# Optimization experiments

Hardware: AMD Instinct MI355X
Metric: run time of the kernel (lower is better)

The kernel has to match this reference:

```python
import jax, jax.numpy as jnp
import numpy as np

B, W, IN, H, Z, D, OUT, K = 256, 128, 128, 1024, 128, 1024, 128, 3


def _gru_cell(h, x, Wih, Whh, bih, bhh):
    # torch nn.GRU single-layer cell, gate order (r, z, n)
    gi = x @ Wih.T + bih
    gh = h @ Whh.T + bhh
    ir, iz, inn = jnp.split(gi, 3, axis=-1)
    hr, hz, hn = jnp.split(gh, 3, axis=-1)
    r = jax.nn.sigmoid(ir + hr)
    u = jax.nn.sigmoid(iz + hz)
    n = jnp.tanh(inn + r * hn)
    return (1.0 - u) * n + u * h


def setup_inputs():
    key = jax.random.key(0)
    ks = iter(jax.random.split(key, 40))

    def w(shape, fanin):
        return jax.random.normal(next(ks), shape, jnp.float32) / np.float32(np.sqrt(fanin))

    return dict(
        x=jax.random.normal(next(ks), (B, W, IN), jnp.float32),
        eps_q=jax.random.uniform(next(ks), (B, W, Z), jnp.float32),
        eps_p=jax.random.uniform(next(ks), (B, W, OUT), jnp.float32),
        Wih_q=w((3 * H, IN), IN), Whh_q=w((3 * H, H), H),
        bih_q=jnp.zeros(3 * H, jnp.float32), bhh_q=jnp.zeros(3 * H, jnp.float32),
        Wd_q=w((D, Z + H), Z + H), bd_q=jnp.zeros(D, jnp.float32),
        Wmu_q=w((Z, D), D), bmu_q=jnp.zeros(Z, jnp.float32),
        Wsig_q=w((Z, D), D), bsig_q=jnp.zeros(Z, jnp.float32),
        Wp=w((K, Z, Z), Z), bp=jnp.zeros((K, Z), jnp.float32),
        up=0.1 * jax.random.normal(next(ks), (K,), jnp.float32),
        Wlg=w((Z, Z), Z), blg=jnp.zeros(Z, jnp.float32),
        Wih_p=w((3 * H, Z), Z), Whh_p=w((3 * H, H), H),
        bih_p=jnp.zeros(3 * H, jnp.float32), bhh_p=jnp.zeros(3 * H, jnp.float32),
        Wd_p=w((D, H), H), bd_p=jnp.zeros(D, jnp.float32),
        Wmu_p=w((OUT, D), D), bmu_p=jnp.zeros(OUT, jnp.float32),
        Wsig_p=w((OUT, D), D), bsig_p=jnp.zeros(OUT, jnp.float32),
    )


def _forward(x, eps_q, eps_p, Wih_q, Whh_q, bih_q, bhh_q, Wd_q, bd_q, Wmu_q, bmu_q,
             Wsig_q, bsig_q, Wp, bp, up, Wlg, blg, Wih_p, Whh_p, bih_p, bhh_p,
             Wd_p, bd_p, Wmu_p, bmu_p, Wsig_p, bsig_p):
    Bsz = x.shape[0]

    # ---- Qnet: sequential encoder with planar flows ----
    def q_step(carry, inp):
        e, z_prev = carry
        x_t, eps_t = inp  # [B,IN], [B,Z]
        e = _gru_cell(e, x_t, Wih_q, Whh_q, bih_q, bhh_q)
        d = jnp.concatenate([z_prev, e], axis=-1) @ Wd_q.T + bd_q
        mu = d @ Wmu_q.T + bmu_q
        logvar = jax.nn.softplus(d @ Wsig_q.T + bsig_q)
        z = mu + jnp.exp(0.5 * logvar) * eps_t
        for k in range(K):  # planar normalizing flows: z + u * tanh(Wz + b)
            z = z + up[k] * jnp.tanh(z @ Wp[k].T + bp[k])
        return (e, z), (z, mu, logvar)

    e0 = jnp.zeros((Bsz, H), x.dtype)
    z0 = jnp.zeros((Bsz, Z), x.dtype)
    _, (z_seq, mu_seq, lv_seq) = jax.lax.scan(
        q_step, (e0, z0), (jnp.swapaxes(x, 0, 1), jnp.swapaxes(eps_q, 0, 1)))

    # ---- Pnet: sequential decoder ----
    def p_step(d_t, inp):
        z_t, eps_t = inp
        zt = z_t @ Wlg.T + blg  # LGSSM linear
        d_t = _gru_cell(d_t, zt, Wih_p, Whh_p, bih_p, bhh_p)
        dd = d_t @ Wd_p.T + bd_p
        mu = dd @ Wmu_p.T + bmu_p
        sigma = jax.nn.softplus(dd @ Wsig_p.T + bsig_p)
        return d_t, mu + sigma * eps_t

    d0 = jnp.zeros((Bsz, H), x.dtype)
    _, out_seq = jax.lax.scan(p_step, d0, (z_seq, jnp.swapaxes(eps_p, 0, 1)))

    return (jnp.swapaxes(out_seq, 0, 1),
            jnp.swapaxes(mu_seq, 0, 1),
            jnp.swapaxes(lv_seq, 0, 1))


def reference(x, eps_q, eps_p, Wih_q, Whh_q, bih_q, bhh_q, Wd_q, bd_q, Wmu_q, bmu_q,
              Wsig_q, bsig_q, Wp, bp, up, Wlg, blg, Wih_p, Whh_p, bih_p, bhh_p,
              Wd_p, bd_p, Wmu_p, bmu_p, Wsig_p, bsig_p):
    return _forward(x, eps_q, eps_p, Wih_q, Whh_q, bih_q, bhh_q, Wd_q, bd_q, Wmu_q,
                    bmu_q, Wsig_q, bsig_q, Wp, bp, up, Wlg, blg, Wih_p, Whh_p,
                    bih_p, bhh_p, Wd_p, bd_p, Wmu_p, bmu_p, Wsig_p, bsig_p)
```

## Files before the change

### kernel.cpp

```cpp
#include <hip/hip_runtime.h>


typedef __bf16 bf16;
typedef __bf16 bf16x4 __attribute__((ext_vector_type(4)));
typedef __bf16 bf16x8 __attribute__((ext_vector_type(8)));
typedef float  f32x4  __attribute__((ext_vector_type(4)));
typedef unsigned long long u64;
typedef unsigned u32;

static constexpr int CB   = 256;
static constexpr int CW   = 128;
static constexpr int CIN  = 128;
static constexpr int CH   = 1024;
static constexpr int CZ   = 128;
static constexpr int CD   = 1024;
static constexpr int COUT = 128;

static constexpr int APITCH     = 1160;
static constexpr int ABUF_BYTES = 16 * APITCH * 2;
static constexpr int REDN       = 8 * 16 * 17;
static constexpr int RED2_BYTES = 2 * REDN * 4;
static constexpr int FLOW_BYTES = (2 * CZ + 2 * 2 * CZ) * 4;
static constexpr int SMEM_BYTES = ABUF_BYTES + RED2_BYTES + FLOW_BYTES;

#define DEV static __device__ __forceinline__

DEV float sigmoidf_(float x) { return 1.0f / (1.0f + expf(-x)); }
DEV float softplusf_(float x) { return x > 20.0f ? x : log1pf(expf(x)); }
DEV bf16x8 ldfrag(const bf16* p) { return *reinterpret_cast<const bf16x8*>(p); }

#define MFMA(a, b, c) __builtin_amdgcn_mfma_f32_16x16x32_bf16((a), (b), (c), 0, 0, 0)

DEV u64 lda8(const void* p) {
    return __hip_atomic_load((const u64*)p, __ATOMIC_RELAXED, __HIP_MEMORY_SCOPE_AGENT);
}
DEV u32 lda4(const void* p) {
    return __hip_atomic_load((const u32*)p, __ATOMIC_RELAXED, __HIP_MEMORY_SCOPE_AGENT);
}
DEV void sta4(void* p, u32 v) {
    __hip_atomic_store((u32*)p, v, __ATOMIC_RELAXED, __HIP_MEMORY_SCOPE_AGENT);
}
DEV bf16x8 ld_act16(const bf16* p) {
    union { u64 u[2]; bf16x8 v; } r;
    r.u[0] = lda8(p);
    r.u[1] = lda8((const char*)p + 8);
    return r.v;
}
DEV u32 pk2(float a, float b) {
    union { bf16 h[2]; u32 u; } r;
    r.h[0] = (bf16)a; r.h[1] = (bf16)b;
    return r.u;
}

struct Prm {
    const float *eps_q, *eps_p;
    const float *bih_q, *bhh_q, *bd_q, *bmu_q, *bsig_q;
    const float *Wp, *bp, *up, *Wlg, *blg;
    const float *bih_p, *bhh_p, *bd_p, *bmu_p, *bsig_p;
    const bf16 *x_b, *Wih_qb, *Whh_qb, *Wd_qb, *Wmu_qb, *Wsg_qb;
    const bf16 *Wih_pb, *Whh_pb, *Wd_pb, *Wmu_pb, *Wsg_pb;
    float *e_f0, *e_f1; bf16 *e_b0, *e_b1;
    float *d_f0, *d_f1; bf16 *d_b0, *d_b1;
    float *ztmp_f;
    bf16 *dvec_b, *ddvec_b;
    bf16 *zflow;
    bf16 *ztlg;
    u32 *barQ, *barP, *zbar;
    float *out_o, *out_mu, *out_lv;
};

DEV void gbar_h(u32* bar, int wgl, u32 k)
{
    asm volatile("s_waitcnt vmcnt(0)" ::: "memory");
    __syncthreads();
    if (threadIdx.x == 0)
        __hip_atomic_store(&bar[wgl], k, __ATOMIC_RELAXED, __HIP_MEMORY_SCOPE_AGENT);
    if (threadIdx.x < 128) {
        while (__hip_atomic_load(&bar[threadIdx.x], __ATOMIC_RELAXED,
                                 __HIP_MEMORY_SCOPE_AGENT) < k)
            __builtin_amdgcn_s_sleep(1);
    }
    __syncthreads();
}

__global__ void k_cvt(const float* __restrict__ src, bf16* __restrict__ dst, int n)
{
    int i = (blockIdx.x * blockDim.x + threadIdx.x) * 4;
    if (i < n) {
        float4 v = *reinterpret_cast<const float4*>(src + i);
        bf16x4 o;
        o[0] = (bf16)v.x; o[1] = (bf16)v.y; o[2] = (bf16)v.z; o[3] = (bf16)v.w;
        *reinterpret_cast<bf16x4*>(dst + i) = o;
    }
}

DEV void stage_act(bf16* abuf, int tid, int r0,
                   const bf16* __restrict__ head, long hs, int K1, int hagent,
                   const bf16* __restrict__ body, long bs)
{
    const int CHN = (K1 + CH) >> 3;
    const int TOT = 16 * CHN;
    for (int idx = tid; idx < TOT; idx += 512) {
        const int row = idx / CHN;
        const int k = (idx - row * CHN) * 8;
        bf16x8 v;
        if (k < K1) {
            const bf16* s = head + (long)(r0 + row) * hs + k;
            v = hagent ? ld_act16(s) : ldfrag(s);
        } else {
            v = ld_act16(body + (long)(r0 + row) * bs + (k - K1));
        }
        *reinterpret_cast<bf16x8*>(abuf + (long)row * APITCH + k) = v;
    }
    __syncthreads();
}

DEV void gru_compute(const Prm& p, const bf16* abuf, int r0, int n0,
                     int lane, int wave,
                     const bf16* __restrict__ Wih, const bf16* __restrict__ Whh,
                     const float* __restrict__ bih, const float* __restrict__ bhh,
                     const float* __restrict__ Efin,
                     float* __restrict__ Efo, bf16* __restrict__ Ebo)
{
    const int lr = lane & 15, lkE = (lane >> 4) * 8;
    const int c = n0 + wave * 16 + lr;
    const bf16* arow = abuf + (long)lr * APITCH;

    f32x4 acc[4] = {};
#pragma unroll 4
    for (int k = 0; k < CIN; k += 32) {
        bf16x8 a = *reinterpret_cast<const bf16x8*>(arow + k + lkE);
#pragma unroll
        for (int g = 0; g < 3; ++g) {
            bf16x8 b = ldfrag(Wih + ((long)g * CH + c) * CIN + k + lkE);
            const int grp = (g == 2) ? 2 : g;
            acc[grp] = MFMA(a, b, acc[grp]);
        }
    }
#pragma unroll 4
    for (int k = 0; k < CH; k += 32) {
        bf16x8 a = *reinterpret_cast<const bf16x8*>(arow + CIN + k + lkE);
#pragma unroll
        for (int g = 0; g < 3; ++g) {
            bf16x8 b = ldfrag(Whh + ((long)g * CH + c) * CH + k + lkE);
            const int grp = (g == 2) ? 3 : g;
            acc[grp] = MFMA(a, b, acc[grp]);
        }
    }

    const float b0r = bih[c] + bhh[c];
    const float b0z = bih[CH + c] + bhh[CH + c];
    const float bin = bih[2 * CH + c];
    const float bhn = bhh[2 * CH + c];
    const int rbase = r0 + (lane >> 4) * 4;
#pragma unroll
    for (int i = 0; i < 4; ++i) {
        const int row = rbase + i;
        float gr = acc[0][i] + b0r;
        float gz = acc[1][i] + b0z;
        float gi = acc[2][i] + bin;
        float gh = acc[3][i] + bhn;
        float r = sigmoidf_(gr);
        float u = sigmoidf_(gz);
        float n = tanhf(gi + r * gh);
        float en = (1.0f - u) * n + u * Efin[(long)row * CH + c];
        Efo[(long)row * CH + c] = en;
        float vB = __shfl_xor(en, 1);
        if (!(lane & 1))
            sta4(Ebo + (long)row * CH + c, pk2(en, vB));
    }
}

DEV void lin_compute(const bf16* abuf, int r0, int n0, int lane, int wave, int Ktot,
                     const bf16* __restrict__ W,
                     const float* __restrict__ bias, bf16* __restrict__ Out)
{
    const int lr = lane & 15, lkE = (lane >> 4) * 8;
    const int c = n0 + wave * 16 + lr;
    const bf16* arow = abuf + (long)lr * APITCH;
    const bf16* wrow = W + (long)c * Ktot;

    f32x4 acc = {};
#pragma unroll 4
    for (int k = 0; k < CH; k += 32) {
        bf16x8 a = *reinterpret_cast<const bf16x8*>(arow + (Ktot - CH) + k + lkE);
        bf16x8 b = ldfrag(wrow + (Ktot - CH) + k + lkE);
        acc = MFMA(a, b, acc);
    }
    if (Ktot > CH) {
#pragma unroll 4
        for (int k = 0; k < CZ; k += 32) {
            bf16x8 a = *reinterpret_cast<const bf16x8*>(arow + k + lkE);
            bf16x8 b = ldfrag(wrow + k + lkE);
            acc = MFMA(a, b, acc);
        }
    }

    const float bb = bias[c];
    const int rbase = r0 + (lane >> 4) * 4;
#pragma unroll
    for (int i = 0; i < 4; ++i) {
        float v = acc[i] + bb;
        float vB = __shfl_xor(v, 1);
        if (!(lane & 1))
            sta4(Out + (long)(rbase + i) * CD + c, pk2(v, vB));
    }
}

template <int MODE>
DEV void phase_tail2(const Prm& p, int t, int wgl, int tid, int lane, int wave,
                     float* Ra, float* Rs, const bf16* __restrict__ A,
                     const bf16* __restrict__ Wa, const bf16* __restrict__ Wb,
                     const float* __restrict__ ba, const float* __restrict__ bb)
{
    const int lr = lane & 15, lkE = (lane >> 4) * 8;
    const int mb = (wgl >> 3) << 4;
    const int nb = (wgl & 7) << 4;
    f32x4 am = {}, as = {};
    const int k0 = wave * 128;
#pragma unroll
    for (int kk = 0; kk < 128; kk += 32) {
        const int k = k0 + kk;
        bf16x8 a  = ld_act16(A + (long)(mb + lr) * CD + k + lkE);
        bf16x8 bm = ldfrag(Wa + (long)(nb + lr) * CD + k + lkE);
        bf16x8 bs = ldfrag(Wb + (long)(nb + lr) * CD + k + lkE);
        am = MFMA(a, bm, am);
        as = MFMA(a, bs, as);
    }
    __syncthreads();
#pragma unroll
    for (int i = 0; i < 4; ++i) {
        Ra[(wave * 16 + (lane >> 4) * 4 + i) * 17 + lr] = am[i];
        Rs[(wave * 16 + (lane >> 4) * 4 + i) * 17 + lr] = as[i];
    }
    __syncthreads();
    if (tid < 256) {
        const int trow = tid >> 4, tcol = tid & 15;
        float vm = 0.f, vs = 0.f;
#pragma unroll
        for (int w = 0; w < 8; ++w) {
            vm += Ra[(w * 16 + trow) * 17 + tcol];
            vs += Rs[(w * 16 + trow) * 17 + tcol];
        }
        const int row = mb + trow, col = nb + tcol;
        if constexpr (MODE == 0) {
            float mu = vm + ba[col];
            float lv = softplusf_(vs + bb[col]);
            float e  = p.eps_q[(long)row * CW * CZ + (long)t * CZ + col];
            float z  = mu + expf(0.5f * lv) * e;
            p.out_mu[(long)row * CW * CZ + (long)t * CZ + col] = mu;
            p.out_lv[(long)row * CW * CZ + (long)t * CZ + col] = lv;
            sta4(p.ztmp_f + (long)row * CZ + col, __float_as_uint(z));
        } else {
            float m  = vm + ba[col];
            float sg = softplusf_(vs + bb[col]);
            float e  = p.eps_p[(long)row * CW * COUT + (long)t * COUT + col];
            p.out_o[(long)row * CW * COUT + (long)t * COUT + col] = m + sg * e;
        }
    }
}

DEV void phase_flows2(const Prm& p, int wgl, int tid, int t, float* zl, float* ps)
{
    const int rg = tid >> 8;
    const int sub = tid & 255;
    const int c = sub & 127, half = sub >> 7;
    const int row = wgl * 2 + rg;
    float* zrow = zl + rg * CZ;
    float* pall = ps + rg * 2 * CZ;

    if (half == 0)
        zrow[c] = __uint_as_float(lda4(p.ztmp_f + (long)row * CZ + c));
    __syncthreads();

#pragma unroll 1
    for (int kf = 0; kf < 3; ++kf) {
        const float* wr = p.Wp + ((long)kf * CZ + c) * CZ + half * 64;
        const float* zh = zrow + half * 64;
        float s = 0.f;
#pragma unroll
        for (int j = 0; j < 64; j += 4) {
            float4 w = *reinterpret_cast<const float4*>(wr + j);
            s += zh[j] * w.x + zh[j + 1] * w.y + zh[j + 2] * w.z + zh[j + 3] * w.w;
        }
        pall[half * CZ + c] = s;
        __syncthreads();
        if (half == 0) {
            float sf = pall[c] + pall[CZ + c] + p.bp[kf * CZ + c];
            zrow[c] += p.up[kf] * tanhf(sf);
        }
        __syncthreads();
    }
    {
        const float* wr = p.Wlg + (long)c * CZ + half * 64;
        const float* zh = zrow + half * 64;
        float s = 0.f;
#pragma unroll
        for (int j = 0; j < 64; j += 4) {
            float4 w = *reinterpret_cast<const float4*>(wr + j);
            s += zh[j] * w.x + zh[j + 1] * w.y + zh[j + 2] * w.z + zh[j + 3] * w.w;
        }
        pall[half * CZ + c] = s;
        __syncthreads();
        if (half == 0) {
            float zt = pall[c] + pall[CZ + c] + p.blg[c];
            float ztB = __shfl_xor(zt, 1);
            if (!(c & 1)) {
                sta4(p.ztlg  + ((size_t)t * CB + row) * CZ + c, pk2(zt, ztB));
                sta4(p.zflow + ((size_t)(t + 1) * CB + row) * CZ + c,
                     pk2(zrow[c], zrow[c + 1]));
            }
        }
    }
}

__launch_bounds__(512)
__global__ void mega(Prm p)
{
    extern __shared__ char smem[];
    bf16*  abuf = (bf16*)smem;
    float* Ra   = (float*)(smem + ABUF_BYTES);
    float* Rs   = Ra + REDN;
    float* ZLp  = (float*)(smem + ABUF_BYTES + RED2_BYTES);
    float* PSp  = ZLp + 2 * CZ;

    const int wg = blockIdx.x, tid = threadIdx.x;
    const int lane = tid & 63, wave = tid >> 6;
    const bool isQ = wg < 128;
    const int wgl = isQ ? wg : wg - 128;
    const int r0 = (wgl >> 3) * 16;
    const int n0 = (wgl & 7) * 128;

    if (isQ) {
        u32 bk = 0;
#pragma unroll 1
        for (int t = 0; t < CW; ++t) {
            const int bi = t & 1;
            const bf16*  eb_i = bi ? p.e_b1 : p.e_b0;
            const float* ef_i = bi ? p.e_f1 : p.e_f0;
            bf16*  eb_o = bi ? p.e_b0 : p.e_b1;
            float* ef_o = bi ? p.e_f0 : p.e_f1;

            stage_act(abuf, tid, r0, p.x_b + (long)t * CIN, (long)CW * CIN, CIN, 0,
                      eb_i, CH);
            gru_compute(p, abuf, r0, n0, lane, wave, p.Wih_qb, p.Whh_qb,
                        p.bih_q, p.bhh_q, ef_i, ef_o, eb_o);
            gbar_h(p.barQ, wgl, ++bk);
            stage_act(abuf, tid, r0, p.zflow + (size_t)t * CB * CZ, CZ, CZ, 1,
                      eb_o, CH);
            lin_compute(abuf, r0, n0, lane, wave, CZ + CH, p.Wd_qb, p.bd_q, p.dvec_b);
            gbar_h(p.barQ, wgl, ++bk);
            phase_tail2<0>(p, t, wgl, tid, lane, wave, Ra, Rs,
                           p.dvec_b, p.Wmu_qb, p.Wsg_qb, p.bmu_q, p.bsig_q);
            gbar_h(p.barQ, wgl, ++bk);
            phase_flows2(p, wgl, tid, t, ZLp, PSp);
            asm volatile("s_waitcnt vmcnt(0)" ::: "memory");
            __syncthreads();
            if (tid == 0)
                __hip_atomic_store(&p.zbar[wgl], (u32)(t + 1),
                                   __ATOMIC_RELAXED, __HIP_MEMORY_SCOPE_AGENT);
            __syncthreads();
        }
    } else {
        u32 bk = 0;
#pragma unroll 1
        for (int t = 0; t < CW; ++t) {
            if (tid < 128) {
                while (__hip_atomic_load(&p.zbar[tid], __ATOMIC_RELAXED,
                                         __HIP_MEMORY_SCOPE_AGENT) < (u32)(t + 1))
                    __builtin_amdgcn_s_sleep(2);
            }
            __syncthreads();

            const int bi = t & 1;
            const bf16*  db_i = bi ? p.d_b1 : p.d_b0;
            const float* df_i = bi ? p.d_f1 : p.d_f0;
            bf16*  db_o = bi ? p.d_b0 : p.d_b1;
            float* df_o = bi ? p.d_f0 : p.d_f1;

            stage_act(abuf, tid, r0, p.ztlg + (size_t)t * CB * CZ, CZ, CZ, 1,
                      db_i, CH);
            gru_compute(p, abuf, r0, n0, lane, wave, p.Wih_pb, p.Whh_pb,
                        p.bih_p, p.bhh_p, df_i, df_o, db_o);
            gbar_h(p.barP, wgl, ++bk);
            stage_act(abuf, tid, r0, nullptr, 0, 0, 0, db_o, CH);
            lin_compute(abuf, r0, n0, lane, wave, CH, p.Wd_pb, p.bd_p, p.ddvec_b);
            gbar_h(p.barP, wgl, ++bk);
            phase_tail2<1>(p, t, wgl, tid, lane, wave, Ra, Rs,
                           p.ddvec_b, p.Wmu_pb, p.Wsg_pb, p.bmu_p, p.bsig_p);
        }
    }
}

extern "C" void kernel_launch(void* const* d_in, const int* in_sizes, int n_in,
                              void* d_out, int out_size, void* d_ws, size_t ws_size,
                              hipStream_t stream)
{
    Prm p;
    const float* x      = (const float*)d_in[0];
    p.eps_q  = (const float*)d_in[1];
    p.eps_p  = (const float*)d_in[2];
    const float* Wih_q  = (const float*)d_in[3];
    const float* Whh_q  = (const float*)d_in[4];
    p.bih_q  = (const float*)d_in[5];
    p.bhh_q  = (const float*)d_in[6];
    const float* Wd_q   = (const float*)d_in[7];
    p.bd_q   = (const float*)d_in[8];
    const float* Wmu_q  = (const float*)d_in[9];
    p.bmu_q  = (const float*)d_in[10];
    const float* Wsig_q = (const float*)d_in[11];
    p.bsig_q = (const float*)d_in[12];
    p.Wp     = (const float*)d_in[13];
    p.bp     = (const float*)d_in[14];
    p.up     = (const float*)d_in[15];
    p.Wlg    = (const float*)d_in[16];
    p.blg    = (const float*)d_in[17];
    const float* Wih_p  = (const float*)d_in[18];
    const float* Whh_p  = (const float*)d_in[19];
    p.bih_p  = (const float*)d_in[20];
    p.bhh_p  = (const float*)d_in[21];
    const float* Wd_p   = (const float*)d_in[22];
    p.bd_p   = (const float*)d_in[23];
    const float* Wmu_p  = (const float*)d_in[24];
    p.bmu_p  = (const float*)d_in[25];
    const float* Wsig_p = (const float*)d_in[26];
    p.bsig_p = (const float*)d_in[27];

    p.out_o  = (float*)d_out;
    p.out_mu = p.out_o + (size_t)CB * CW * COUT;
    p.out_lv = p.out_mu + (size_t)CB * CW * CZ;

    char* wp_ = (char*)d_ws;
    auto carve = [&](size_t bytes) -> void* {
        void* q = (void*)wp_;
        wp_ += (bytes + 255) & ~(size_t)255;
        return q;
    };
    p.e_f0 = (float*)carve((size_t)CB * CH * 4);
    p.e_f1 = (float*)carve((size_t)CB * CH * 4);
    p.e_b0 = (bf16*)carve((size_t)CB * CH * 2);
    p.e_b1 = (bf16*)carve((size_t)CB * CH * 2);
    p.d_f0 = (float*)carve((size_t)CB * CH * 4);
    p.d_f1 = (float*)carve((size_t)CB * CH * 4);
    p.d_b0 = (bf16*)carve((size_t)CB * CH * 2);
    p.d_b1 = (bf16*)carve((size_t)CB * CH * 2);
    p.ztmp_f  = (float*)carve((size_t)CB * CZ * 4);
    p.dvec_b  = (bf16*)carve((size_t)CB * CD * 2);
    p.ddvec_b = (bf16*)carve((size_t)CB * CD * 2);
    p.zflow   = (bf16*)carve((size_t)(CW + 1) * CB * CZ * 2);
    p.ztlg    = (bf16*)carve((size_t)CW * CB * CZ * 2);
    p.barQ    = (u32*)carve(512);
    p.barP    = (u32*)carve(512);
    p.zbar    = (u32*)carve(512);
    bf16* x_b    = (bf16*)carve((size_t)CB * CW * CIN * 2);
    bf16* Wih_qb = (bf16*)carve((size_t)3 * CH * CIN * 2);
    bf16* Whh_qb = (bf16*)carve((size_t)3 * CH * CH * 2);
    bf16* Wd_qb  = (bf16*)carve((size_t)CD * (CZ + CH) * 2);
    bf16* Wmu_qb = (bf16*)carve((size_t)CZ * CD * 2);
    bf16* Wsg_qb = (bf16*)carve((size_t)CZ * CD * 2);
    bf16* Wih_pb = (bf16*)carve((size_t)3 * CH * CZ * 2);
    bf16* Whh_pb = (bf16*)carve((size_t)3 * CH * CH * 2);
    bf16* Wd_pb  = (bf16*)carve((size_t)CD * CH * 2);
    bf16* Wmu_pb = (bf16*)carve((size_t)COUT * CD * 2);
    bf16* Wsg_pb = (bf16*)carve((size_t)COUT * CD * 2);
    p.x_b = x_b;       p.Wih_qb = Wih_qb; p.Whh_qb = Whh_qb;
    p.Wd_qb = Wd_qb;   p.Wmu_qb = Wmu_qb; p.Wsg_qb = Wsg_qb;
    p.Wih_pb = Wih_pb; p.Whh_pb = Whh_pb; p.Wd_pb = Wd_pb;
    p.Wmu_pb = Wmu_pb; p.Wsg_pb = Wsg_pb;

    hipMemsetAsync(p.e_f0, 0, (size_t)CB * CH * 4, stream);
    hipMemsetAsync(p.e_b0, 0, (size_t)CB * CH * 2, stream);
    hipMemsetAsync(p.d_f0, 0, (size_t)CB * CH * 4, stream);
    hipMemsetAsync(p.d_b0, 0, (size_t)CB * CH * 2, stream);
    hipMemsetAsync(p.zflow, 0, (size_t)CB * CZ * 2, stream);
    hipMemsetAsync(p.barQ, 0, 512, stream);
    hipMemsetAsync(p.barP, 0, 512, stream);
    hipMemsetAsync(p.zbar, 0, 512, stream);

    auto cvt = [&](const float* s, bf16* d, size_t n) {
        k_cvt<<<dim3((unsigned)((n / 4 + 255) / 256)), dim3(256), 0, stream>>>(s, d, (int)n);
    };
    cvt(x,      x_b,    (size_t)CB * CW * CIN);
    cvt(Wih_q,  Wih_qb, (size_t)3 * CH * CIN);
    cvt(Whh_q,  Whh_qb, (size_t)3 * CH * CH);
    cvt(Wd_q,   Wd_qb,  (size_t)CD * (CZ + CH));
    cvt(Wmu_q,  Wmu_qb, (size_t)CZ * CD);
    cvt(Wsig_q, Wsg_qb, (size_t)CZ * CD);
    cvt(Wih_p,  Wih_pb, (size_t)3 * CH * CZ);
    cvt(Whh_p,  Whh_pb, (size_t)3 * CH * CH);
    cvt(Wd_p,   Wd_pb,  (size_t)CD * CH);
    cvt(Wmu_p,  Wmu_pb, (size_t)COUT * CD);
    cvt(Wsig_p, Wsg_pb, (size_t)COUT * CD);

    mega<<<dim3(256), dim3(512), SMEM_BYTES, stream>>>(p);
}
```

Before: 9.720 ms.

## Use per-timestep write-once activation buffers so reads can use cached loads

When the workspace is large enough, hidden states, intermediate vectors, z samples and LGSSM outputs are kept in per-timestep slices rather than ping-pong buffers. Each slice is then written only once, so consumers can use ordinary cached fragment loads instead of coherent agent-scope loads. This is meant to cut the latency of cross-workgroup activation reads inside the persistent recurrent kernel. In exchange it uses much more workspace memory, falls back to the old path when the workspace is small, and relies on the cached reads never seeing stale lines. The convert kernel also switches to packed stores.

Result: slower. 10.68 ms (+9.9%).

```diff
diff --git a/kernel.cpp b/kernel.cpp
--- a/kernel.cpp
+++ b/kernel.cpp
@@ -59,14 +59,15 @@
     const float *bih_p, *bhh_p, *bd_p, *bmu_p, *bsig_p;
     const bf16 *x_b, *Wih_qb, *Whh_qb, *Wd_qb, *Wmu_qb, *Wsg_qb;
     const bf16 *Wih_pb, *Whh_pb, *Wd_pb, *Wmu_pb, *Wsg_pb;
-    float *e_f0, *e_f1; bf16 *e_b0, *e_b1;
-    float *d_f0, *d_f1; bf16 *d_b0, *d_b1;
-    float *ztmp_f;
-    bf16 *dvec_b, *ddvec_b;
-    bf16 *zflow;
-    bf16 *ztlg;
+    float *e_f0, *e_f1, *d_f0, *d_f1;
+    bf16 *e_h, *d_h;
+    bf16 *dvec_h, *ddvec_h;
+    float *ztmp_h;
+    bf16 *zflow_h;
+    bf16 *ztlg_h;
     u32 *barQ, *barP, *zbar;
     float *out_o, *out_mu, *out_lv;
+    int big;
 };
 
 DEV void gbar_h(u32* bar, int wgl, u32 k)
@@ -88,15 +89,14 @@
     int i = (blockIdx.x * blockDim.x + threadIdx.x) * 4;
     if (i < n) {
         float4 v = *reinterpret_cast<const float4*>(src + i);
-        bf16x4 o;
-        o[0] = (bf16)v.x; o[1] = (bf16)v.y; o[2] = (bf16)v.z; o[3] = (bf16)v.w;
-        *reinterpret_cast<bf16x4*>(dst + i) = o;
+        *reinterpret_cast<u32*>(dst + i)     = pk2(v.x, v.y);
+        *reinterpret_cast<u32*>(dst + i + 2) = pk2(v.z, v.w);
     }
 }
 
 DEV void stage_act(bf16* abuf, int tid, int r0,
-                   const bf16* __restrict__ head, long hs, int K1, int hagent,
-                   const bf16* __restrict__ body, long bs)
+                   const bf16* head, long hs, int K1, bool hc,
+                   const bf16* body, long bs, bool bc)
 {
     const int CHN = (K1 + CH) >> 3;
     const int TOT = 16 * CHN;
@@ -106,17 +106,17 @@
         bf16x8 v;
         if (k < K1) {
             const bf16* s = head + (long)(r0 + row) * hs + k;
-            v = hagent ? ld_act16(s) : ldfrag(s);
+            v = hc ? ldfrag(s) : ld_act16(s);
         } else {
-            v = ld_act16(body + (long)(r0 + row) * bs + (k - K1));
+            const bf16* s = body + (long)(r0 + row) * bs + (k - K1);
+            v = bc ? ldfrag(s) : ld_act16(s);
         }
         *reinterpret_cast<bf16x8*>(abuf + (long)row * APITCH + k) = v;
     }
     __syncthreads();
 }
 
-DEV void gru_compute(const Prm& p, const bf16* abuf, int r0, int n0,
-                     int lane, int wave,
+DEV void gru_compute(const bf16* abuf, int r0, int n0, int lane, int wave,
                      const bf16* __restrict__ Wih, const bf16* __restrict__ Whh,
                      const float* __restrict__ bih, const float* __restrict__ bhh,
                      const float* __restrict__ Efin,
@@ -156,13 +156,9 @@
 #pragma unroll
     for (int i = 0; i < 4; ++i) {
         const int row = rbase + i;
-        float gr = acc[0][i] + b0r;
-        float gz = acc[1][i] + b0z;
-        float gi = acc[2][i] + bin;
-        float gh = acc[3][i] + bhn;
-        float r = sigmoidf_(gr);
-        float u = sigmoidf_(gz);
-        float n = tanhf(gi + r * gh);
+        float r = sigmoidf_(acc[0][i] + b0r);
+        float u = sigmoidf_(acc[1][i] + b0z);
+        float n = tanhf(acc[2][i] + bin + r * (acc[3][i] + bhn));
         float en = (1.0f - u) * n + u * Efin[(long)row * CH + c];
         Efo[(long)row * CH + c] = en;
         float vB = __shfl_xor(en, 1);
@@ -210,6 +206,7 @@
 template <int MODE>
 DEV void phase_tail2(const Prm& p, int t, int wgl, int tid, int lane, int wave,
                      float* Ra, float* Rs, const bf16* __restrict__ A,
+                     float* __restrict__ ztmp,
                      const bf16* __restrict__ Wa, const bf16* __restrict__ Wb,
                      const float* __restrict__ ba, const float* __restrict__ bb)
 {
@@ -218,14 +215,26 @@
     const int nb = (wgl & 7) << 4;
     f32x4 am = {}, as = {};
     const int k0 = wave * 128;
-#pragma unroll
-    for (int kk = 0; kk < 128; kk += 32) {
-        const int k = k0 + kk;
-        bf16x8 a  = ld_act16(A + (long)(mb + lr) * CD + k + lkE);
-        bf16x8 bm = ldfrag(Wa + (long)(nb + lr) * CD + k + lkE);
-        bf16x8 bs = ldfrag(Wb + (long)(nb + lr) * CD + k + lkE);
-        am = MFMA(a, bm, am);
-        as = MFMA(a, bs, as);
+    if (p.big) {
+#pragma unroll
+        for (int kk = 0; kk < 128; kk += 32) {
+            const int k = k0 + kk;
+            bf16x8 a  = ldfrag(A + (long)(mb + lr) * CD + k + lkE);
+            bf16x8 bm = ldfrag(Wa + (long)(nb + lr) * CD + k + lkE);
+            bf16x8 bs = ldfrag(Wb + (long)(nb + lr) * CD + k + lkE);
+            am = MFMA(a, bm, am);
+            as = MFMA(a, bs, as);
+        }
+    } else {
+#pragma unroll
+        for (int kk = 0; kk < 128; kk += 32) {
+            const int k = k0 + kk;
+            bf16x8 a  = ld_act16(A + (long)(mb + lr) * CD + k + lkE);
+            bf16x8 bm = ldfrag(Wa + (long)(nb + lr) * CD + k + lkE);
+            bf16x8 bs = ldfrag(Wb + (long)(nb + lr) * CD + k + lkE);
+            am = MFMA(a, bm, am);
+            as = MFMA(a, bs, as);
+        }
     }
     __syncthreads();
 #pragma unroll
@@ -250,7 +259,7 @@
             float z  = mu + expf(0.5f * lv) * e;
             p.out_mu[(long)row * CW * CZ + (long)t * CZ + col] = mu;
             p.out_lv[(long)row * CW * CZ + (long)t * CZ + col] = lv;
-            sta4(p.ztmp_f + (long)row * CZ + col, __float_as_uint(z));
+            sta4(ztmp + (long)row * CZ + col, __float_as_uint(z));
         } else {
             float m  = vm + ba[col];
             float sg = softplusf_(vs + bb[col]);
@@ -260,7 +269,9 @@
     }
 }
 
-DEV void phase_flows2(const Prm& p, int wgl, int tid, int t, float* zl, float* ps)
+DEV void phase_flows2(const Prm& p, int wgl, int tid, int t, float* zl, float* ps,
+                      const float* __restrict__ ztmp,
+                      bf16* __restrict__ ztlg, bf16* __restrict__ zflow_next)
 {
     const int rg = tid >> 8;
     const int sub = tid & 255;
@@ -270,7 +281,8 @@
     float* pall = ps + rg * 2 * CZ;
 
     if (half == 0)
-        zrow[c] = __uint_as_float(lda4(p.ztmp_f + (long)row * CZ + c));
+        zrow[c] = p.big ? ztmp[(long)row * CZ + c]
+                        : __uint_as_float(lda4(ztmp + (long)row * CZ + c));
     __syncthreads();
 
 #pragma unroll 1
@@ -306,9 +318,8 @@
             float zt = pall[c] + pall[CZ + c] + p.blg[c];
             float ztB = __shfl_xor(zt, 1);
             if (!(c & 1)) {
-                sta4(p.ztlg  + ((size_t)t * CB + row) * CZ + c, pk2(zt, ztB));
-                sta4(p.zflow + ((size_t)(t + 1) * CB + row) * CZ + c,
-                     pk2(zrow[c], zrow[c + 1]));
+                sta4(ztlg + (long)row * CZ + c, pk2(zt, ztB));
+                sta4(zflow_next + (long)row * CZ + c, pk2(zrow[c], zrow[c + 1]));
             }
         }
     }
@@ -330,30 +341,39 @@
     const int wgl = isQ ? wg : wg - 128;
     const int r0 = (wgl >> 3) * 16;
     const int n0 = (wgl & 7) * 128;
+    const bool big = p.big != 0;
+    const size_t SH = (size_t)CB * CH;
+    const size_t SD = (size_t)CB * CD;
+    const size_t SZ = (size_t)CB * CZ;
 
     if (isQ) {
         u32 bk = 0;
 #pragma unroll 1
         for (int t = 0; t < CW; ++t) {
-            const int bi = t & 1;
-            const bf16*  eb_i = bi ? p.e_b1 : p.e_b0;
-            const float* ef_i = bi ? p.e_f1 : p.e_f0;
-            bf16*  eb_o = bi ? p.e_b0 : p.e_b1;
-            float* ef_o = bi ? p.e_f0 : p.e_f1;
-
-            stage_act(abuf, tid, r0, p.x_b + (long)t * CIN, (long)CW * CIN, CIN, 0,
-                      eb_i, CH);
-            gru_compute(p, abuf, r0, n0, lane, wave, p.Wih_qb, p.Whh_qb,
-                        p.bih_q, p.bhh_q, ef_i, ef_o, eb_o);
+            const int sIn  = big ? t : (t & 1);
+            const int sOut = big ? (t + 1) : ((t + 1) & 1);
+            const int sT   = big ? t : 0;
+            const float* ef_i = (t & 1) ? p.e_f1 : p.e_f0;
+            float*       ef_o = (t & 1) ? p.e_f0 : p.e_f1;
+
+            stage_act(abuf, tid, r0, p.x_b + (long)t * CIN, (long)CW * CIN, CIN, true,
+                      p.e_h + (size_t)sIn * SH, CH, big);
+            gru_compute(abuf, r0, n0, lane, wave, p.Wih_qb, p.Whh_qb,
+                        p.bih_q, p.bhh_q, ef_i, ef_o, p.e_h + (size_t)sOut * SH);
             gbar_h(p.barQ, wgl, ++bk);
-            stage_act(abuf, tid, r0, p.zflow + (size_t)t * CB * CZ, CZ, CZ, 1,
-                      eb_o, CH);
-            lin_compute(abuf, r0, n0, lane, wave, CZ + CH, p.Wd_qb, p.bd_q, p.dvec_b);
+            stage_act(abuf, tid, r0, p.zflow_h + (size_t)sIn * SZ, CZ, CZ, big,
+                      p.e_h + (size_t)sOut * SH, CH, big);
+            lin_compute(abuf, r0, n0, lane, wave, CZ + CH, p.Wd_qb, p.bd_q,
+                        p.dvec_h + (size_t)sT * SD);
             gbar_h(p.barQ, wgl, ++bk);
             phase_tail2<0>(p, t, wgl, tid, lane, wave, Ra, Rs,
-                           p.dvec_b, p.Wmu_qb, p.Wsg_qb, p.bmu_q, p.bsig_q);
+                           p.dvec_h + (size_t)sT * SD, p.ztmp_h + (size_t)sT * SZ,
+                           p.Wmu_qb, p.Wsg_qb, p.bmu_q, p.bsig_q);
             gbar_h(p.barQ, wgl, ++bk);
-            phase_flows2(p, wgl, tid, t, ZLp, PSp);
+            phase_flows2(p, wgl, tid, t, ZLp, PSp,
+                         p.ztmp_h + (size_t)sT * SZ,
+                         p.ztlg_h + (size_t)(big ? t : (t & 1)) * SZ,
+                         p.zflow_h + (size_t)sOut * SZ);
             asm volatile("s_waitcnt vmcnt(0)" ::: "memory");
             __syncthreads();
             if (tid == 0)
@@ -372,22 +392,26 @@
             }
             __syncthreads();
 
-            const int bi = t & 1;
-            const bf16*  db_i = bi ? p.d_b1 : p.d_b0;
-            const float* df_i = bi ? p.d_f1 : p.d_f0;
-            bf16*  db_o = bi ? p.d_b0 : p.d_b1;
-            float* df_o = bi ? p.d_f0 : p.d_f1;
-
-            stage_act(abuf, tid, r0, p.ztlg + (size_t)t * CB * CZ, CZ, CZ, 1,
-                      db_i, CH);
-            gru_compute(p, abuf, r0, n0, lane, wave, p.Wih_pb, p.Whh_pb,
-                        p.bih_p, p.bhh_p, df_i, df_o, db_o);
+            const int sIn  = big ? t : (t & 1);
+            const int sOut = big ? (t + 1) : ((t + 1) & 1);
+            const int sT   = big ? t : 0;
+            const float* df_i = (t & 1) ? p.d_f1 : p.d_f0;
+            float*       df_o = (t & 1) ? p.d_f0 : p.d_f1;
+
+            stage_act(abuf, tid, r0,
+                      p.ztlg_h + (size_t)(big ? t : (t & 1)) * SZ, CZ, CZ, big,
+                      p.d_h + (size_t)sIn * SH, CH, big);
+            gru_compute(abuf, r0, n0, lane, wave, p.Wih_pb, p.Whh_pb,
+                        p.bih_p, p.bhh_p, df_i, df_o, p.d_h + (size_t)sOut * SH);
             gbar_h(p.barP, wgl, ++bk);
-            stage_act(abuf, tid, r0, nullptr, 0, 0, 0, db_o, CH);
-            lin_compute(abuf, r0, n0, lane, wave, CH, p.Wd_pb, p.bd_p, p.ddvec_b);
+            stage_act(abuf, tid, r0, nullptr, 0, 0, false,
+                      p.d_h + (size_t)sOut * SH, CH, big);
+            lin_compute(abuf, r0, n0, lane, wave, CH, p.Wd_pb, p.bd_p,
+                        p.ddvec_h + (size_t)sT * SD);
             gbar_h(p.barP, wgl, ++bk);
             phase_tail2<1>(p, t, wgl, tid, lane, wave, Ra, Rs,
-                           p.ddvec_b, p.Wmu_pb, p.Wsg_pb, p.bmu_p, p.bsig_p);
+                           p.ddvec_h + (size_t)sT * SD, nullptr,
+                           p.Wmu_pb, p.Wsg_pb, p.bmu_p, p.bsig_p);
         }
     }
 }
@@ -430,6 +454,11 @@
     p.out_mu = p.out_o + (size_t)CB * CW * COUT;
     p.out_lv = p.out_mu + (size_t)CB * CW * CZ;
 
+    p.big = (ws_size >= (size_t)340 * 1024 * 1024) ? 1 : 0;
+    const int NS = p.big ? (CW + 1) : 2;
+    const int NT = p.big ? CW : 1;
+    const int NZ = p.big ? CW : 2;
+
     char* wp_ = (char*)d_ws;
     auto carve = [&](size_t bytes) -> void* {
         void* q = (void*)wp_;
@@ -438,17 +467,15 @@
     };
     p.e_f0 = (float*)carve((size_t)CB * CH * 4);
     p.e_f1 = (float*)carve((size_t)CB * CH * 4);
-    p.e_b0 = (bf16*)carve((size_t)CB * CH * 2);
-    p.e_b1 = (bf16*)carve((size_t)CB * CH * 2);
     p.d_f0 = (float*)carve((size_t)CB * CH * 4);
     p.d_f1 = (float*)carve((size_t)CB * CH * 4);
-    p.d_b0 = (bf16*)carve((size_t)CB * CH * 2);
-    p.d_b1 = (bf16*)carve((size_t)CB * CH * 2);
-    p.ztmp_f  = (float*)carve((size_t)CB * CZ * 4);
-    p.dvec_b  = (bf16*)carve((size_t)CB * CD * 2);
-    p.ddvec_b = (bf16*)carve((size_t)CB * CD * 2);
-    p.zflow   = (bf16*)carve((size_t)(CW + 1) * CB * CZ * 2);
-    p.ztlg    = (bf16*)carve((size_t)CW * CB * CZ * 2);
+    p.e_h     = (bf16*)carve((size_t)NS * CB * CH * 2);
+    p.d_h     = (bf16*)carve((size_t)NS * CB * CH * 2);
+    p.dvec_h  = (bf16*)carve((size_t)NT * CB * CD * 2);
+    p.ddvec_h = (bf16*)carve((size_t)NT * CB * CD * 2);
+    p.ztmp_h  = (float*)carve((size_t)NT * CB * CZ * 4);
+    p.zflow_h = (bf16*)carve((size_t)NS * CB * CZ * 2);
+    p.ztlg_h  = (bf16*)carve((size_t)NZ * CB * CZ * 2);
     p.barQ    = (u32*)carve(512);
     p.barP    = (u32*)carve(512);
     p.zbar    = (u32*)carve(512);
@@ -469,10 +496,10 @@
     p.Wmu_pb = Wmu_pb; p.Wsg_pb = Wsg_pb;
 
     hipMemsetAsync(p.e_f0, 0, (size_t)CB * CH * 4, stream);
-    hipMemsetAsync(p.e_b0, 0, (size_t)CB * CH * 2, stream);
     hipMemsetAsync(p.d_f0, 0, (size_t)CB * CH * 4, stream);
-    hipMemsetAsync(p.d_b0, 0, (size_t)CB * CH * 2, stream);
-    hipMemsetAsync(p.zflow, 0, (size_t)CB * CZ * 2, stream);
+    hipMemsetAsync(p.e_h, 0, (size_t)CB * CH * 2, stream);
+    hipMemsetAsync(p.d_h, 0, (size_t)CB * CH * 2, stream);
+    hipMemsetAsync(p.zflow_h, 0, (size_t)CB * CZ * 2, stream);
     hipMemsetAsync(p.barQ, 0, 512, stream);
     hipMemsetAsync(p.barP, 0, 512, stream);
     hipMemsetAsync(p.zbar, 0, 512, stream);
```
